# Kernel tuning notes

Measured on AMD Instinct MI355X. Metric: run time of the kernel, lower is better.

## Reference

```python
import jax, jax.numpy as jnp
import numpy as np

BL = 5
N_SC = 2 ** BL  # 32; LUT A assumed to be the exact product table A[i,j] = i*j
T, B, NT, C, H = 4, 16, 196, 384, 12
TAU, ALPHA = 2.0, 4.0  # LIF tau, surrogate sigmoid alpha (spikingjelly default)


def _clean(t):
    t = jnp.where(jnp.isnan(t), 0.0, t)
    return jnp.where(jnp.isinf(t), 1.0, t)


def _pow2_scale(m):
    # 2 ** int(log2(int(N_SC / m))), with m==0 -> 1 guard, as in SC_MAT_MAC_p
    m = jnp.where(m == 0, 1.0, m)
    return 2.0 ** jnp.floor(jnp.log2(jnp.floor(N_SC / m)))


def sc_linear(x, W, b):
    # Forward value = SC LUT-quantized matmul; gradient = dense linear (out.data = p
    # in torch leaves autograd on nn.Linear) -> straight-through estimator.
    a, w, c = _clean(x), _clean(W), _clean(b)
    SN2 = _pow2_scale(jnp.max(jnp.abs(a)))
    SN1 = _pow2_scale(jnp.maximum(jnp.max(jnp.abs(w)), jnp.max(jnp.abs(c))))
    aa = jnp.trunc(a * SN2)   # .int() truncates toward zero
    bb = jnp.trunc(w * SN1)
    cc = jnp.trunc(c * SN1)
    # LUT gather A[|aa|,|bb|] with sign correction, summed over K == aa @ bb.T
    # (A[i,j] = i*j), computed without materializing the (M*O*K) intermediate.
    x9 = aa @ bb.T
    p = (jnp.trunc(x9 / SN2) + cc) / SN1
    lin = x @ W.T + b
    return lin + jax.lax.stop_gradient(p - lin)


def batch_norm(x, gamma, beta):
    # training-mode batch stats over the flattened (T*B*N) token dim, eps=1e-5
    mean = x.mean(0)
    var = ((x - mean) ** 2).mean(0)
    return gamma * (x - mean) / jnp.sqrt(var + 1e-5) + beta


def lif(x_seq, v_th=1.0):
    # Multi-step LIF, v_reset=0, hard reset, detach_reset, sigmoid surrogate
    def step(v, x):
        v = v + (x - v) / TAU
        u = v - v_th
        sg = jax.nn.sigmoid(ALPHA * u)
        spike = sg + jax.lax.stop_gradient((u >= 0).astype(x.dtype) - sg)
        v = v * (1.0 - jax.lax.stop_gradient(spike))
        return v, spike
    _, s = jax.lax.scan(step, jnp.zeros_like(x_seq[0]), x_seq)
    return s


def setup_inputs() -> dict:
    key = jax.random.key(0)
    ks = jax.random.split(key, 20)
    lim = 1.0 / np.sqrt(C)
    inp = {"x": jax.random.normal(ks[0], (T, B, NT, C), jnp.float32)}
    for i, n in enumerate(["q", "k", "v", "p"]):
        inp["W" + n] = jax.random.uniform(ks[1 + 4 * i], (C, C), jnp.float32, -lim, lim)
        inp["b" + n] = jax.random.uniform(ks[2 + 4 * i], (C,), jnp.float32, -lim, lim)
        inp["g" + n] = jnp.ones((1, C), jnp.float32)
        inp["beta" + n] = jnp.zeros((1, C), jnp.float32)
    return inp


def reference(x, Wq, bq, gq, betaq, Wk, bk, gk, betak, Wv, bv, gv, betav, Wp, bp, gp, betap):
    Tn, Bn, Nt, Cn = x.shape
    d = Cn // H
    xf = x.reshape(-1, Cn)

    def qkv(W, b, g, be):
        o = batch_norm(sc_linear(xf, W, b), g, be)
        o = lif(o.reshape(Tn, Bn, Nt, Cn))
        return o.reshape(Tn, Bn, Nt, H, d).transpose(0, 1, 3, 2, 4)  # t b h n d

    q = qkv(Wq, bq, gq, betaq)
    k = qkv(Wk, bk, gk, betak)
    v = qkv(Wv, bv, gv, betav)
    attn = jnp.einsum('tbhnd,tbhmd->tbhnm', q, k) * 0.125
    y = jnp.einsum('tbhnm,tbhmd->tbhnd', attn, v)
    y = y.transpose(0, 1, 3, 2, 4).reshape(Tn, Bn, Nt, Cn)
    y = lif(y, v_th=0.5)  # attn_lif
    o = batch_norm(sc_linear(y.reshape(-1, Cn), Wp, bp), gp, betap).reshape(Tn, Bn, Nt, Cn)
    return lif(o)
```

## Files before the change

kernel.cpp:

```cpp
#include <hip/hip_runtime.h>
#include <hip/hip_bf16.h>
#include <stdint.h>

#define T_   4
#define B_   16
#define NT_  196
#define C_   384
#define H_   12
#define M_   12544
#define PBUF_ELEMS 4816896

typedef __attribute__((ext_vector_type(8))) short bf16x8;
typedef __attribute__((ext_vector_type(4))) float f32x4;

__device__ __forceinline__ void gload_lds16(const void* g, void* l) {
  typedef __attribute__((address_space(1))) const unsigned int GU32;
  typedef __attribute__((address_space(3))) unsigned int LU32;
  __builtin_amdgcn_global_load_lds((GU32*)g, (LU32*)l, 16, 0, 0);
}

__device__ __forceinline__ short f2bf_bits(float f) {
  __hip_bfloat16 h = __float2bfloat16(f);
  return *(short*)&h;
}

__global__ __launch_bounds__(64) void init_slots_kernel(unsigned* slots) {
  if (threadIdx.x < 16) slots[threadIdx.x] = 0u;
}

__global__ __launch_bounds__(256) void absmax_kernel(const float* __restrict__ x, int n,
                                                     unsigned* __restrict__ slot) {
  float m = 0.f;
  for (long i = (long)blockIdx.x * 256 + threadIdx.x; i < n; i += (long)gridDim.x * 256)
    m = fmaxf(m, fabsf(x[i]));
#pragma unroll
  for (int o = 32; o > 0; o >>= 1) m = fmaxf(m, __shfl_down(m, o));
  __shared__ float sm[4];
  int wid = threadIdx.x >> 6, lane = threadIdx.x & 63;
  if (lane == 0) sm[wid] = m;
  __syncthreads();
  if (threadIdx.x == 0) {
    m = fmaxf(fmaxf(sm[0], sm[1]), fmaxf(sm[2], sm[3]));
    atomicMax(slot, __float_as_uint(m));
  }
}

__global__ void scales_kernel(const unsigned* __restrict__ slots, float* __restrict__ SC) {
  if (threadIdx.x == 0 && blockIdx.x == 0) {
    for (int i = 0; i < 5; ++i) {
      float m = __uint_as_float(slots[i]);
      if (m == 0.f) m = 1.f;
      float q = floorf(32.f / m);
      float sn = 0.f;
      if (q >= 1.f) { unsigned qi = (unsigned)q; sn = (float)(1u << (31 - __clz((int)qi))); }
      SC[i] = sn;
    }
    SC[5] = 32.f;
  }
}

__global__ __launch_bounds__(256) void quant_x_kernel(const float* __restrict__ x,
                                                      const float* __restrict__ SC,
                                                      short* __restrict__ xq) {
  const float sn2 = SC[0];
  size_t i = ((size_t)blockIdx.x * 256 + threadIdx.x) * 4;
  float4 v = *reinterpret_cast<const float4*>(x + i);
  short4 o;
  o.x = f2bf_bits(truncf(v.x * sn2));
  o.y = f2bf_bits(truncf(v.y * sn2));
  o.z = f2bf_bits(truncf(v.z * sn2));
  o.w = f2bf_bits(truncf(v.w * sn2));
  *reinterpret_cast<short4*>(xq + i) = o;
}

__global__ __launch_bounds__(256) void quant_w_kernel(const float* __restrict__ W,
                                                      const float* __restrict__ bias,
                                                      const float* __restrict__ SC, int sn1_slot,
                                                      short* __restrict__ wq, float* __restrict__ ccq) {
  const float sn1 = SC[sn1_slot];
  int gid = blockIdx.x * 256 + threadIdx.x;
  wq[gid] = f2bf_bits(truncf(W[gid] * sn1));
  if (gid < C_) ccq[gid] = truncf(bias[gid] * sn1);
}

__global__ __launch_bounds__(256) void mfma_gemm_kernel(
    const short* __restrict__ Aq, const short* __restrict__ Bq,
    const float* __restrict__ cc, const float* __restrict__ SC,
    int sn2_slot, int sn1_slot,
    float* __restrict__ out, long long* __restrict__ part) {
  __shared__ short As[8192];
  __shared__ short Bs[8192];
  __shared__ unsigned long long sred[128][2];
  const int tid = threadIdx.x;
  const int lane = tid & 63;
  const int wid = tid >> 6;
  const int wm = wid >> 1, wn = wid & 1;
  const int m0 = blockIdx.x * 128;
  const int n0 = blockIdx.y * 128;
  if (tid < 128) { sred[tid][0] = 0ull; sred[tid][1] = 0ull; }
  f32x4 acc[4][4];
#pragma unroll
  for (int i = 0; i < 4; ++i)
#pragma unroll
    for (int j = 0; j < 4; ++j) acc[i][j] = (f32x4){0.f, 0.f, 0.f, 0.f};

  for (int k0 = 0; k0 < C_; k0 += 64) {
#pragma unroll
    for (int p = 0; p < 4; ++p) {
      int o = p * 4096 + tid * 16;
      int row = o >> 7;
      int slot = (o >> 4) & 7;
      int hs = slot ^ (row & 7);
      int ldsoff = p * 4096 + (tid & ~63) * 16;
      gload_lds16(Aq + (size_t)(m0 + row) * C_ + k0 + hs * 8, (char*)As + ldsoff);
      gload_lds16(Bq + (size_t)(n0 + row) * C_ + k0 + hs * 8, (char*)Bs + ldsoff);
    }
    __syncthreads();
#pragma unroll
    for (int kk = 0; kk < 2; ++kk) {
      bf16x8 af[4], bfr[4];
#pragma unroll
      for (int i = 0; i < 4; ++i) {
        int r = wm * 64 + i * 16 + (lane & 15);
        int h = kk * 4 + (lane >> 4);
        af[i] = *(const bf16x8*)((const char*)As + r * 128 + ((h ^ (r & 7)) << 4));
        int c = wn * 64 + i * 16 + (lane & 15);
        bfr[i] = *(const bf16x8*)((const char*)Bs + c * 128 + ((h ^ (c & 7)) << 4));
      }
#pragma unroll
      for (int i = 0; i < 4; ++i)
#pragma unroll
        for (int j = 0; j < 4; ++j)
          acc[i][j] = __builtin_amdgcn_mfma_f32_16x16x32_bf16(af[i], bfr[j], acc[i][j], 0, 0, 0);
    }
    __syncthreads();
  }
  const float SN2 = SC[sn2_slot], SN1 = SC[sn1_slot];
  const float invSN2 = 1.0f / SN2, invSN1 = 1.0f / SN1;
  long long s1[4] = {0, 0, 0, 0}, s2[4] = {0, 0, 0, 0};
#pragma unroll
  for (int j = 0; j < 4; ++j) {
    int gcol = n0 + wn * 64 + j * 16 + (lane & 15);
    float ccv = cc[gcol];
#pragma unroll
    for (int i = 0; i < 4; ++i) {
#pragma unroll
      for (int r = 0; r < 4; ++r) {
        int grow = m0 + wm * 64 + i * 16 + (lane >> 4) * 4 + r;
        float qf = truncf(acc[i][j][r] * invSN2) + ccv;
        out[(size_t)grow * C_ + gcol] = qf * invSN1;
        long long qi = (long long)qf;
        s1[j] += qi; s2[j] += qi * qi;
      }
    }
  }
#pragma unroll
  for (int j = 0; j < 4; ++j) {
    s1[j] += __shfl_xor(s1[j], 16); s1[j] += __shfl_xor(s1[j], 32);
    s2[j] += __shfl_xor(s2[j], 16); s2[j] += __shfl_xor(s2[j], 32);
  }
  if (lane < 16) {
#pragma unroll
    for (int j = 0; j < 4; ++j) {
      int cl = wn * 64 + j * 16 + lane;
      atomicAdd(&sred[cl][0], (unsigned long long)s1[j]);
      atomicAdd(&sred[cl][1], (unsigned long long)s2[j]);
    }
  }
  __syncthreads();
  if (tid < 128) {
    part[((size_t)blockIdx.x * C_ + n0 + tid) * 2 + 0] = (long long)sred[tid][0];
    part[((size_t)blockIdx.x * C_ + n0 + tid) * 2 + 1] = (long long)sred[tid][1];
  }
}

__global__ __launch_bounds__(384) void stats_final_kernel(
    const long long* __restrict__ part, const float* __restrict__ SC, int sn1_slot,
    float* __restrict__ bn) {
  int c = threadIdx.x;
  long long S1 = 0, S2 = 0;
  for (int b = 0; b < 98; ++b) {
    S1 += part[((size_t)b * C_ + c) * 2 + 0];
    S2 += part[((size_t)b * C_ + c) * 2 + 1];
  }
  double inv = 1.0 / (double)SC[sn1_slot];
  double s = (double)S1 * inv;
  double s2 = (double)S2 * inv * inv;
  double mean = s / (double)M_;
  float m32 = (float)mean;
  double md = (double)m32;
  double var = (s2 - 2.0 * md * s + (double)M_ * md * md) / (double)M_;
  float v32 = (float)var;
  bn[c * 2 + 0] = m32;
  bn[c * 2 + 1] = sqrtf(v32 + 1e-5f);
}

__device__ __forceinline__ float lif_step(float& v, float x, float vth) {
  v = v + (x - v) * 0.5f;
  float u = v - vth;
  float spike = (u >= 0.0f) ? 1.0f : 0.0f;
  v = (u >= 0.0f) ? 0.0f : v;
  return spike;
}

__global__ __launch_bounds__(384) void bn_lif_pack_kernel(
    const float* __restrict__ pbuf, const float* __restrict__ bn,
    const float* __restrict__ g, const float* __restrict__ beta,
    uint32_t* __restrict__ pack) {
  int c = threadIdx.x;
  int n = blockIdx.x;
  int b = blockIdx.y;
  float mean = bn[c * 2 + 0], sd = bn[c * 2 + 1];
  float gg = g[c], bb = beta[c];
  int h = c >> 5;
  float v = 0.f;
  for (int t = 0; t < T_; ++t) {
    size_t row = (size_t)(t * B_ + b) * NT_ + n;
    float p = pbuf[row * C_ + c];
    float o = (gg * (p - mean)) / sd + bb;
    float spike = lif_step(v, o, 1.0f);
    unsigned long long m = __ballot(spike != 0.0f);
    if ((c & 31) == 0) {
      uint32_t part_ = (c & 32) ? (uint32_t)(m >> 32) : (uint32_t)m;
      pack[((size_t)(t * B_ + b) * H_ + h) * NT_ + n] = part_;
    }
  }
}

__global__ __launch_bounds__(256) void attn_fused_kernel(
    const uint32_t* __restrict__ qp, const uint32_t* __restrict__ kp,
    const uint32_t* __restrict__ vp, short* __restrict__ yq) {
  __shared__ uint32_t qs[256], ksm[256], vsm[256];
  __shared__ uint32_t kT[32][8], vT[32][8];
  __shared__ int Z[32][32];
  const int bh = blockIdx.x;
  const int b = bh / H_, h = bh % H_;
  const int tid = threadIdx.x, lane = tid & 63, w = tid >> 6;
  const int d = tid & 31, nn = tid >> 5;
  float vst[25];
#pragma unroll
  for (int i = 0; i < 25; ++i) vst[i] = 0.f;
  const short one32 = f2bf_bits(32.f);
  const short zer = f2bf_bits(0.f);
  for (int t = 0; t < T_; ++t) {
    size_t base = ((size_t)(t * B_ + b) * H_ + h) * NT_;
    qs[tid]  = (tid < NT_) ? qp[base + tid] : 0u;
    ksm[tid] = (tid < NT_) ? kp[base + tid] : 0u;
    vsm[tid] = (tid < NT_) ? vp[base + tid] : 0u;
    __syncthreads();
    uint32_t km = ksm[w * 64 + lane], vm = vsm[w * 64 + lane];
#pragma unroll
    for (int j = 0; j < 32; ++j) {
      unsigned long long bk = __ballot((km >> j) & 1u);
      unsigned long long bv = __ballot((vm >> j) & 1u);
      if (lane == 0) {
        kT[j][2 * w] = (uint32_t)bk; kT[j][2 * w + 1] = (uint32_t)(bk >> 32);
        vT[j][2 * w] = (uint32_t)bv; vT[j][2 * w + 1] = (uint32_t)(bv >> 32);
      }
    }
    __syncthreads();
    for (int pz = tid; pz < 1024; pz += 256) {
      int j = pz >> 5, dd = pz & 31;
      int z = 0;
#pragma unroll
      for (int ww = 0; ww < 8; ++ww) z += __popc(kT[j][ww] & vT[dd][ww]);
      Z[j][dd] = z;
    }
    __syncthreads();
    int zc[32];
#pragma unroll
    for (int j = 0; j < 32; ++j) zc[j] = Z[j][d];
#pragma unroll
    for (int i = 0; i < 25; ++i) {
      int n = i * 8 + nn;
      if (n < NT_) {
        uint32_t qm = qs[n];
        int a = 0;
#pragma unroll
        for (int j = 0; j < 32; ++j) a += ((qm >> j) & 1u) ? zc[j] : 0;
        float y = 0.125f * (float)a;
        float v = vst[i];
        v = v + (y - v) * 0.5f;
        short outv;
        if (v - 0.5f >= 0.f) { v = 0.f; outv = one32; } else { outv = zer; }
        vst[i] = v;
        yq[((size_t)(t * B_ + b) * NT_ + n) * C_ + h * 32 + d] = outv;
      }
    }
    __syncthreads();
  }
}

__global__ __launch_bounds__(384) void bn_lif_out_kernel(
    const float* __restrict__ p2, const float* __restrict__ bn,
    const float* __restrict__ g, const float* __restrict__ beta,
    float* __restrict__ out) {
  int c = threadIdx.x, n = blockIdx.x, b = blockIdx.y;
  float mean = bn[c * 2 + 0], sd = bn[c * 2 + 1];
  float gg = g[c], bb = beta[c];
  float v = 0.f;
  for (int t = 0; t < T_; ++t) {
    size_t idx = ((size_t)(t * B_ + b) * NT_ + n) * C_ + c;
    float o = (gg * (p2[idx] - mean)) / sd + bb;
    out[idx] = lif_step(v, o, 1.0f);
  }
}

extern "C" void kernel_launch(void* const* d_in, const int* in_sizes, int n_in,
                              void* d_out, int out_size, void* d_ws, size_t ws_size,
                              hipStream_t stream) {
  (void)in_sizes; (void)n_in; (void)out_size; (void)ws_size;
  const float* x = (const float*)d_in[0];
  const float* W[4]  = {(const float*)d_in[1],  (const float*)d_in[5],
                        (const float*)d_in[9],  (const float*)d_in[13]};
  const float* bv[4] = {(const float*)d_in[2],  (const float*)d_in[6],
                        (const float*)d_in[10], (const float*)d_in[14]};
  const float* g[4]  = {(const float*)d_in[3],  (const float*)d_in[7],
                        (const float*)d_in[11], (const float*)d_in[15]};
  const float* be[4] = {(const float*)d_in[4],  (const float*)d_in[8],
                        (const float*)d_in[12], (const float*)d_in[16]};
  float* out = (float*)d_out;

  char* ws = (char*)d_ws;
  unsigned*  slots = (unsigned*)(ws + 0);
  float*     SC    = (float*)(ws + 64);
  float*     bnp   = (float*)(ws + 128);
  float*     ccq   = (float*)(ws + 16384);
  long long* part  = (long long*)(ws + 32768);
  uint32_t*  pack  = (uint32_t*)(ws + 0x260000);
  short*     wq    = (short*)(ws + 0x420000);
  short*     xq    = (short*)(ws + 0x550000);
  short*     yq    = (short*)(ws + 0xE80000);
  float*     pbuf  = (float*)(ws + 0x17B0000);
  const size_t PPS = (size_t)98 * C_ * 2;

  init_slots_kernel<<<1, 64, 0, stream>>>(slots);
  absmax_kernel<<<1024, 256, 0, stream>>>(x, PBUF_ELEMS, slots + 0);
  for (int s = 0; s < 4; ++s) {
    absmax_kernel<<<64, 256, 0, stream>>>(W[s], C_ * C_, slots + 1 + s);
    absmax_kernel<<<1, 256, 0, stream>>>(bv[s], C_, slots + 1 + s);
  }
  scales_kernel<<<1, 1, 0, stream>>>(slots, SC);

  quant_x_kernel<<<4704, 256, 0, stream>>>(x, SC, xq);
  for (int s = 0; s < 4; ++s)
    quant_w_kernel<<<576, 256, 0, stream>>>(W[s], bv[s], SC, 1 + s,
                                            wq + (size_t)s * 147456, ccq + s * C_);

  for (int s = 0; s < 3; ++s) {
    mfma_gemm_kernel<<<dim3(98, 3), 256, 0, stream>>>(
        xq, wq + (size_t)s * 147456, ccq + s * C_, SC, 0, 1 + s, pbuf, part + s * PPS);
    stats_final_kernel<<<1, 384, 0, stream>>>(part + s * PPS, SC, 1 + s, bnp + s * C_ * 2);
    bn_lif_pack_kernel<<<dim3(NT_, B_), 384, 0, stream>>>(
        pbuf, bnp + s * C_ * 2, g[s], be[s], pack + (size_t)s * 150528);
  }

  attn_fused_kernel<<<B_ * H_, 256, 0, stream>>>(pack, pack + 150528, pack + 2 * 150528, yq);

  mfma_gemm_kernel<<<dim3(98, 3), 256, 0, stream>>>(
      yq, wq + 3ull * 147456, ccq + 3 * C_, SC, 5, 4, pbuf, part + 3 * PPS);
  stats_final_kernel<<<1, 384, 0, stream>>>(part + 3 * PPS, SC, 4, bnp + 3 * C_ * 2);
  bn_lif_out_kernel<<<dim3(NT_, B_), 384, 0, stream>>>(pbuf, bnp + 3 * C_ * 2, g[3], be[3], out);
}
```

Before: 307.9 us.

## Batch QKV projections into one wide GEMM and split attention into zcalc/apply

The three Q/K/V projection GEMMs become a single 98x9 grid writing a 1152-wide buffer, and their stats and BN/LIF pack passes are likewise merged into one launch each. The absmax and weight-quant launches are batched across the four weights, and the x absmax is vectorised. The 192-block attention kernel is split into a K^T·V popcount kernel with 768 blocks and an apply kernel with a 4-way token chunk, to raise parallelism. The goal is fewer launches and better GPU occupancy, at the cost of extra workspace and a round trip through global memory for Z.

```diff
diff --git a/kernel.cpp b/kernel.cpp
--- a/kernel.cpp
+++ b/kernel.cpp
@@ -8,6 +8,7 @@
 #define C_   384
 #define H_   12
 #define M_   12544
+#define NW_  1152
 #define PBUF_ELEMS 4816896
 
 typedef __attribute__((ext_vector_type(8))) short bf16x8;
@@ -24,15 +25,13 @@
   return *(short*)&h;
 }
 
-__global__ __launch_bounds__(64) void init_slots_kernel(unsigned* slots) {
-  if (threadIdx.x < 16) slots[threadIdx.x] = 0u;
-}
-
-__global__ __launch_bounds__(256) void absmax_kernel(const float* __restrict__ x, int n,
-                                                     unsigned* __restrict__ slot) {
+__global__ __launch_bounds__(256) void absmax_x_kernel(const float* __restrict__ x, int n4,
+                                                       unsigned* __restrict__ slot) {
   float m = 0.f;
-  for (long i = (long)blockIdx.x * 256 + threadIdx.x; i < n; i += (long)gridDim.x * 256)
-    m = fmaxf(m, fabsf(x[i]));
+  for (long i = (long)blockIdx.x * 256 + threadIdx.x; i < n4; i += (long)gridDim.x * 256) {
+    float4 v = reinterpret_cast<const float4*>(x)[i];
+    m = fmaxf(fmaxf(fmaxf(fabsf(v.x), fabsf(v.y)), fmaxf(fabsf(v.z), fabsf(v.w))), m);
+  }
 #pragma unroll
   for (int o = 32; o > 0; o >>= 1) m = fmaxf(m, __shfl_down(m, o));
   __shared__ float sm[4];
@@ -45,8 +44,35 @@
   }
 }
 
-__global__ void scales_kernel(const unsigned* __restrict__ slots, float* __restrict__ SC) {
-  if (threadIdx.x == 0 && blockIdx.x == 0) {
+__global__ __launch_bounds__(256) void absmax_wb_kernel(
+    const float* __restrict__ W0, const float* __restrict__ W1,
+    const float* __restrict__ W2, const float* __restrict__ W3,
+    const float* __restrict__ b0, const float* __restrict__ b1,
+    const float* __restrict__ b2, const float* __restrict__ b3,
+    unsigned* __restrict__ slots) {
+  int s = blockIdx.y;
+  const float* W = (s == 0) ? W0 : (s == 1) ? W1 : (s == 2) ? W2 : W3;
+  const float* bb = (s == 0) ? b0 : (s == 1) ? b1 : (s == 2) ? b2 : b3;
+  float m = 0.f;
+  for (int i = blockIdx.x * 256 + threadIdx.x; i < C_ * C_; i += 64 * 256)
+    m = fmaxf(m, fabsf(W[i]));
+  if (blockIdx.x == 0)
+    for (int i = threadIdx.x; i < C_; i += 256) m = fmaxf(m, fabsf(bb[i]));
+#pragma unroll
+  for (int o = 32; o > 0; o >>= 1) m = fmaxf(m, __shfl_down(m, o));
+  __shared__ float sm[4];
+  int wid = threadIdx.x >> 6, lane = threadIdx.x & 63;
+  if (lane == 0) sm[wid] = m;
+  __syncthreads();
+  if (threadIdx.x == 0) {
+    m = fmaxf(fmaxf(sm[0], sm[1]), fmaxf(sm[2], sm[3]));
+    atomicMax(slots + 1 + s, __float_as_uint(m));
+  }
+}
+
+__global__ __launch_bounds__(64) void scales_kernel(const unsigned* __restrict__ slots,
+                                                    float* __restrict__ SC) {
+  if (threadIdx.x == 0) {
     for (int i = 0; i < 5; ++i) {
       float m = __uint_as_float(slots[i]);
       if (m == 0.f) m = 1.f;
@@ -73,20 +99,25 @@
   *reinterpret_cast<short4*>(xq + i) = o;
 }
 
-__global__ __launch_bounds__(256) void quant_w_kernel(const float* __restrict__ W,
-                                                      const float* __restrict__ bias,
-                                                      const float* __restrict__ SC, int sn1_slot,
-                                                      short* __restrict__ wq, float* __restrict__ ccq) {
-  const float sn1 = SC[sn1_slot];
+__global__ __launch_bounds__(256) void quant_w_kernel(
+    const float* __restrict__ W0, const float* __restrict__ W1,
+    const float* __restrict__ W2, const float* __restrict__ W3,
+    const float* __restrict__ b0, const float* __restrict__ b1,
+    const float* __restrict__ b2, const float* __restrict__ b3,
+    const float* __restrict__ SC, short* __restrict__ wq, float* __restrict__ ccq) {
+  int s = blockIdx.y;
+  const float* W = (s == 0) ? W0 : (s == 1) ? W1 : (s == 2) ? W2 : W3;
+  const float* bb = (s == 0) ? b0 : (s == 1) ? b1 : (s == 2) ? b2 : b3;
+  const float sn1 = SC[1 + s];
   int gid = blockIdx.x * 256 + threadIdx.x;
-  wq[gid] = f2bf_bits(truncf(W[gid] * sn1));
-  if (gid < C_) ccq[gid] = truncf(bias[gid] * sn1);
+  wq[(size_t)s * C_ * C_ + gid] = f2bf_bits(truncf(W[gid] * sn1));
+  if (gid < C_) ccq[s * C_ + gid] = truncf(bb[gid] * sn1);
 }
 
 __global__ __launch_bounds__(256) void mfma_gemm_kernel(
     const short* __restrict__ Aq, const short* __restrict__ Bq,
     const float* __restrict__ cc, const float* __restrict__ SC,
-    int sn2_slot, int sn1_slot,
+    int sn2_slot, int sn1_base, int ldc,
     float* __restrict__ out, long long* __restrict__ part) {
   __shared__ short As[8192];
   __shared__ short Bs[8192];
@@ -135,7 +166,7 @@
     }
     __syncthreads();
   }
-  const float SN2 = SC[sn2_slot], SN1 = SC[sn1_slot];
+  const float SN2 = SC[sn2_slot], SN1 = SC[sn1_base + blockIdx.y / 3];
   const float invSN2 = 1.0f / SN2, invSN1 = 1.0f / SN1;
   long long s1[4] = {0, 0, 0, 0}, s2[4] = {0, 0, 0, 0};
 #pragma unroll
@@ -148,7 +179,7 @@
       for (int r = 0; r < 4; ++r) {
         int grow = m0 + wm * 64 + i * 16 + (lane >> 4) * 4 + r;
         float qf = truncf(acc[i][j][r] * invSN2) + ccv;
-        out[(size_t)grow * C_ + gcol] = qf * invSN1;
+        out[(size_t)grow * ldc + gcol] = qf * invSN1;
         long long qi = (long long)qf;
         s1[j] += qi; s2[j] += qi * qi;
       }
@@ -169,30 +200,29 @@
   }
   __syncthreads();
   if (tid < 128) {
-    part[((size_t)blockIdx.x * C_ + n0 + tid) * 2 + 0] = (long long)sred[tid][0];
-    part[((size_t)blockIdx.x * C_ + n0 + tid) * 2 + 1] = (long long)sred[tid][1];
+    part[((size_t)blockIdx.x * ldc + n0 + tid) * 2 + 0] = (long long)sred[tid][0];
+    part[((size_t)blockIdx.x * ldc + n0 + tid) * 2 + 1] = (long long)sred[tid][1];
   }
 }
 
 __global__ __launch_bounds__(384) void stats_final_kernel(
-    const long long* __restrict__ part, const float* __restrict__ SC, int sn1_slot,
+    const long long* __restrict__ part, const float* __restrict__ SC, int sn1_base, int Ld,
     float* __restrict__ bn) {
-  int c = threadIdx.x;
+  int c = blockIdx.x * 384 + threadIdx.x;
   long long S1 = 0, S2 = 0;
   for (int b = 0; b < 98; ++b) {
-    S1 += part[((size_t)b * C_ + c) * 2 + 0];
-    S2 += part[((size_t)b * C_ + c) * 2 + 1];
-  }
-  double inv = 1.0 / (double)SC[sn1_slot];
+    S1 += part[((size_t)b * Ld + c) * 2 + 0];
+    S2 += part[((size_t)b * Ld + c) * 2 + 1];
+  }
+  double inv = 1.0 / (double)SC[sn1_base + blockIdx.x];
   double s = (double)S1 * inv;
   double s2 = (double)S2 * inv * inv;
   double mean = s / (double)M_;
   float m32 = (float)mean;
   double md = (double)m32;
   double var = (s2 - 2.0 * md * s + (double)M_ * md * md) / (double)M_;
-  float v32 = (float)var;
   bn[c * 2 + 0] = m32;
-  bn[c * 2 + 1] = sqrtf(v32 + 1e-5f);
+  bn[c * 2 + 1] = sqrtf((float)var + 1e-5f);
 }
 
 __device__ __forceinline__ float lif_step(float& v, float x, float vth) {
@@ -205,76 +235,89 @@
 
 __global__ __launch_bounds__(384) void bn_lif_pack_kernel(
     const float* __restrict__ pbuf, const float* __restrict__ bn,
-    const float* __restrict__ g, const float* __restrict__ beta,
+    const float* __restrict__ g0, const float* __restrict__ g1, const float* __restrict__ g2,
+    const float* __restrict__ be0, const float* __restrict__ be1, const float* __restrict__ be2,
     uint32_t* __restrict__ pack) {
   int c = threadIdx.x;
-  int n = blockIdx.x;
-  int b = blockIdx.y;
-  float mean = bn[c * 2 + 0], sd = bn[c * 2 + 1];
-  float gg = g[c], bb = beta[c];
+  int n = blockIdx.x, b = blockIdx.y, z = blockIdx.z;
+  const float* g  = (z == 0) ? g0 : (z == 1) ? g1 : g2;
+  const float* be = (z == 0) ? be0 : (z == 1) ? be1 : be2;
+  int cg = z * C_ + c;
+  float mean = bn[cg * 2 + 0], sd = bn[cg * 2 + 1];
+  float gg = g[c], bb = be[c];
   int h = c >> 5;
   float v = 0.f;
+  uint32_t* pko = pack + (size_t)z * (T_ * B_ * H_ * NT_);
   for (int t = 0; t < T_; ++t) {
     size_t row = (size_t)(t * B_ + b) * NT_ + n;
-    float p = pbuf[row * C_ + c];
+    float p = pbuf[row * NW_ + cg];
     float o = (gg * (p - mean)) / sd + bb;
     float spike = lif_step(v, o, 1.0f);
     unsigned long long m = __ballot(spike != 0.0f);
     if ((c & 31) == 0) {
-      uint32_t part_ = (c & 32) ? (uint32_t)(m >> 32) : (uint32_t)m;
-      pack[((size_t)(t * B_ + b) * H_ + h) * NT_ + n] = part_;
-    }
-  }
-}
-
-__global__ __launch_bounds__(256) void attn_fused_kernel(
-    const uint32_t* __restrict__ qp, const uint32_t* __restrict__ kp,
-    const uint32_t* __restrict__ vp, short* __restrict__ yq) {
-  __shared__ uint32_t qs[256], ksm[256], vsm[256];
+      uint32_t pt = (c & 32) ? (uint32_t)(m >> 32) : (uint32_t)m;
+      pko[((size_t)(t * B_ + b) * H_ + h) * NT_ + n] = pt;
+    }
+  }
+}
+
+__global__ __launch_bounds__(256) void zcalc_kernel(
+    const uint32_t* __restrict__ kp, const uint32_t* __restrict__ vp,
+    int* __restrict__ zbuf) {
   __shared__ uint32_t kT[32][8], vT[32][8];
-  __shared__ int Z[32][32];
-  const int bh = blockIdx.x;
+  const int tbh = blockIdx.x;
+  const int tid = threadIdx.x, lane = tid & 63, w = tid >> 6;
+  size_t base = (size_t)tbh * NT_;
+  uint32_t km = (tid < NT_) ? kp[base + tid] : 0u;
+  uint32_t vm = (tid < NT_) ? vp[base + tid] : 0u;
+#pragma unroll
+  for (int j = 0; j < 32; ++j) {
+    unsigned long long bk = __ballot((km >> j) & 1u);
+    unsigned long long bv = __ballot((vm >> j) & 1u);
+    if (lane == 0) {
+      kT[j][2 * w] = (uint32_t)bk; kT[j][2 * w + 1] = (uint32_t)(bk >> 32);
+      vT[j][2 * w] = (uint32_t)bv; vT[j][2 * w + 1] = (uint32_t)(bv >> 32);
+    }
+  }
+  __syncthreads();
+  int* Zg = zbuf + (size_t)tbh * 1024;
+  for (int pz = tid; pz < 1024; pz += 256) {
+    int j = pz >> 5, dd = pz & 31;
+    int z = 0;
+#pragma unroll
+    for (int ww = 0; ww < 8; ++ww) z += __popc(kT[j][ww] & vT[dd][ww]);
+    Zg[pz] = z;
+  }
+}
+
+__global__ __launch_bounds__(256) void attn_apply_kernel(
+    const uint32_t* __restrict__ qp, const int* __restrict__ zbuf,
+    short* __restrict__ yq) {
+  __shared__ int Zs[32][32];
+  const int bh = blockIdx.x, chunk = blockIdx.y;
   const int b = bh / H_, h = bh % H_;
-  const int tid = threadIdx.x, lane = tid & 63, w = tid >> 6;
+  const int tid = threadIdx.x;
   const int d = tid & 31, nn = tid >> 5;
-  float vst[25];
-#pragma unroll
-  for (int i = 0; i < 25; ++i) vst[i] = 0.f;
   const short one32 = f2bf_bits(32.f);
   const short zer = f2bf_bits(0.f);
+  float vst[7];
+#pragma unroll
+  for (int i = 0; i < 7; ++i) vst[i] = 0.f;
   for (int t = 0; t < T_; ++t) {
-    size_t base = ((size_t)(t * B_ + b) * H_ + h) * NT_;
-    qs[tid]  = (tid < NT_) ? qp[base + tid] : 0u;
-    ksm[tid] = (tid < NT_) ? kp[base + tid] : 0u;
-    vsm[tid] = (tid < NT_) ? vp[base + tid] : 0u;
-    __syncthreads();
-    uint32_t km = ksm[w * 64 + lane], vm = vsm[w * 64 + lane];
-#pragma unroll
-    for (int j = 0; j < 32; ++j) {
-      unsigned long long bk = __ballot((km >> j) & 1u);
-      unsigned long long bv = __ballot((vm >> j) & 1u);
-      if (lane == 0) {
-        kT[j][2 * w] = (uint32_t)bk; kT[j][2 * w + 1] = (uint32_t)(bk >> 32);
-        vT[j][2 * w] = (uint32_t)bv; vT[j][2 * w + 1] = (uint32_t)(bv >> 32);
-      }
-    }
-    __syncthreads();
-    for (int pz = tid; pz < 1024; pz += 256) {
-      int j = pz >> 5, dd = pz & 31;
-      int z = 0;
-#pragma unroll
-      for (int ww = 0; ww < 8; ++ww) z += __popc(kT[j][ww] & vT[dd][ww]);
-      Z[j][dd] = z;
-    }
+    int tbh = (t * B_ + b) * H_ + h;
+    const int* Zp = zbuf + (size_t)tbh * 1024;
+    for (int i = tid; i < 1024; i += 256) ((int*)Zs)[i] = Zp[i];
     __syncthreads();
     int zc[32];
 #pragma unroll
-    for (int j = 0; j < 32; ++j) zc[j] = Z[j][d];
-#pragma unroll
-    for (int i = 0; i < 25; ++i) {
-      int n = i * 8 + nn;
-      if (n < NT_) {
-        uint32_t qm = qs[n];
+    for (int j = 0; j < 32; ++j) zc[j] = Zs[j][d];
+    size_t qbase = (size_t)tbh * NT_;
+#pragma unroll
+    for (int i = 0; i < 7; ++i) {
+      int no = i * 8 + nn;
+      if (no < 49) {
+        int n = chunk * 49 + no;
+        uint32_t qm = qp[qbase + n];
         int a = 0;
 #pragma unroll
         for (int j = 0; j < 32; ++j) a += ((qm >> j) & 1u) ? zc[j] : 0;
@@ -323,42 +366,41 @@
 
   char* ws = (char*)d_ws;
   unsigned*  slots = (unsigned*)(ws + 0);
-  float*     SC    = (float*)(ws + 64);
-  float*     bnp   = (float*)(ws + 128);
-  float*     ccq   = (float*)(ws + 16384);
-  long long* part  = (long long*)(ws + 32768);
-  uint32_t*  pack  = (uint32_t*)(ws + 0x260000);
-  short*     wq    = (short*)(ws + 0x420000);
-  short*     xq    = (short*)(ws + 0x550000);
-  short*     yq    = (short*)(ws + 0xE80000);
-  float*     pbuf  = (float*)(ws + 0x17B0000);
-  const size_t PPS = (size_t)98 * C_ * 2;
-
-  init_slots_kernel<<<1, 64, 0, stream>>>(slots);
-  absmax_kernel<<<1024, 256, 0, stream>>>(x, PBUF_ELEMS, slots + 0);
-  for (int s = 0; s < 4; ++s) {
-    absmax_kernel<<<64, 256, 0, stream>>>(W[s], C_ * C_, slots + 1 + s);
-    absmax_kernel<<<1, 256, 0, stream>>>(bv[s], C_, slots + 1 + s);
-  }
-  scales_kernel<<<1, 1, 0, stream>>>(slots, SC);
+  float*     SC    = (float*)(ws + 0x40);
+  float*     bnp   = (float*)(ws + 0x80);
+  float*     bn2   = (float*)(ws + 0x6000);
+  float*     ccq   = (float*)(ws + 0x8000);
+  long long* part  = (long long*)(ws + 0x10000);
+  long long* part2 = (long long*)(ws + 0x200000);
+  uint32_t*  pack  = (uint32_t*)(ws + 0x300000);
+  int*       zbuf  = (int*)(ws + 0x500000);
+  short*     wq    = (short*)(ws + 0x800000);
+  short*     xq    = (short*)(ws + 0xA00000);
+  short*     yq    = (short*)(ws + 0x1400000);
+  float*     pwide = (float*)(ws + 0x1E00000);
+  float*     pbuf2 = (float*)(ws + 0x5600000);
+
+  hipMemsetAsync(slots, 0, 64, stream);
+  absmax_x_kernel<<<512, 256, 0, stream>>>(x, PBUF_ELEMS / 4, slots + 0);
+  absmax_wb_kernel<<<dim3(64, 4), 256, 0, stream>>>(
+      W[0], W[1], W[2], W[3], bv[0], bv[1], bv[2], bv[3], slots);
+  scales_kernel<<<1, 64, 0, stream>>>(slots, SC);
 
   quant_x_kernel<<<4704, 256, 0, stream>>>(x, SC, xq);
-  for (int s = 0; s < 4; ++s)
-    quant_w_kernel<<<576, 256, 0, stream>>>(W[s], bv[s], SC, 1 + s,
-                                            wq + (size_t)s * 147456, ccq + s * C_);
-
-  for (int s = 0; s < 3; ++s) {
-    mfma_gemm_kernel<<<dim3(98, 3), 256, 0, stream>>>(
-        xq, wq + (size_t)s * 147456, ccq + s * C_, SC, 0, 1 + s, pbuf, part + s * PPS);
-    stats_final_kernel<<<1, 384, 0, stream>>>(part + s * PPS, SC, 1 + s, bnp + s * C_ * 2);
-    bn_lif_pack_kernel<<<dim3(NT_, B_), 384, 0, stream>>>(
-        pbuf, bnp + s * C_ * 2, g[s], be[s], pack + (size_t)s * 150528);
-  }
-
-  attn_fused_kernel<<<B_ * H_, 256, 0, stream>>>(pack, pack + 150528, pack + 2 * 150528, yq);
+  quant_w_kernel<<<dim3(576, 4), 256, 0, stream>>>(
+      W[0], W[1], W[2], W[3], bv[0], bv[1], bv[2], bv[3], SC, wq, ccq);
+
+  mfma_gemm_kernel<<<dim3(98, 9), 256, 0, stream>>>(
+      xq, wq, ccq, SC, 0, 1, NW_, pwide, part);
+  stats_final_kernel<<<3, 384, 0, stream>>>(part, SC, 1, NW_, bnp);
+  bn_lif_pack_kernel<<<dim3(NT_, B_, 3), 384, 0, stream>>>(
+      pwide, bnp, g[0], g[1], g[2], be[0], be[1], be[2], pack);
+
+  zcalc_kernel<<<T_ * B_ * H_, 256, 0, stream>>>(pack + 150528, pack + 2 * 150528, zbuf);
+  attn_apply_kernel<<<dim3(B_ * H_, 4), 256, 0, stream>>>(pack, zbuf, yq);
 
   mfma_gemm_kernel<<<dim3(98, 3), 256, 0, stream>>>(
-      yq, wq + 3ull * 147456, ccq + 3 * C_, SC, 5, 4, pbuf, part + 3 * PPS);
-  stats_final_kernel<<<1, 384, 0, stream>>>(part + 3 * PPS, SC, 4, bnp + 3 * C_ * 2);
-  bn_lif_out_kernel<<<dim3(NT_, B_), 384, 0, stream>>>(pbuf, bnp + 3 * C_ * 2, g[3], be[3], out);
-}
+      yq, wq + 3ull * C_ * C_, ccq + 3 * C_, SC, 5, 4, C_, pbuf2, part2);
+  stats_final_kernel<<<1, 384, 0, stream>>>(part2, SC, 4, C_, bn2);
+  bn_lif_out_kernel<<<dim3(NT_, B_), 384, 0, stream>>>(pbuf2, bn2, g[3], be[3], out);
+}
```

After: 252.3 us. 1.22x faster.
